# Performance work log

Measured on AMD Instinct MI355X. Metric: run time of the kernel, lower is better.

Reference implementation:

```python
import jax, jax.numpy as jnp
import numpy as np

N, D, G, H, M = 500000, 128, 64, 128, 256  # bag size, local_dim, global_dim, attn_hidden, mlp_hidden
TEMP = 1.0


def setup_inputs() -> dict:
    key = jax.random.key(0)
    ks = jax.random.split(key, 8)
    s = 0.05
    return {
        "bag": jax.random.normal(ks[0], (N, D), jnp.float32),
        "global_feat": jax.random.normal(ks[1], (G,), jnp.float32),
        # attention_V: Linear(D, H) + Tanh
        "Wv": jax.random.normal(ks[2], (H, D), jnp.float32) * s,
        "bv": jnp.zeros((H,), jnp.float32),
        # attention_U: Linear(D, H) + Sigmoid
        "Wu": jax.random.normal(ks[3], (H, D), jnp.float32) * s,
        "bu": jnp.zeros((H,), jnp.float32),
        # attention_weights: Linear(H, 1)
        "Ww": jax.random.normal(ks[4], (1, H), jnp.float32) * s,
        "bw": jnp.zeros((1,), jnp.float32),
        "W1": jax.random.normal(ks[5], (M, D + G), jnp.float32) * s,
        "b1": jnp.zeros((M,), jnp.float32),
        "W2": jax.random.normal(ks[6], (1, M), jnp.float32) * s,
        "b2": jnp.zeros((1,), jnp.float32),
    }


def reference(bag, global_feat, Wv, bv, Wu, bu, Ww, bw, W1, b1, W2, b2):
    # feature_extractor = Identity (use_feature_extractor=False); dropout = identity (eval)
    V = jnp.tanh(bag @ Wv.T + bv)            # [N, H]
    U = jax.nn.sigmoid(bag @ Wu.T + bu)      # [N, H]
    Ggate = V * U                            # [N, H]
    A_raw = Ggate @ Ww.T + bw                # [N, 1]
    alpha = jax.nn.softmax(A_raw / TEMP, axis=0)  # softmax over bag dim
    bag_embedding = alpha.T @ bag            # [1, D]
    fused = jnp.concatenate([bag_embedding, global_feat.reshape(1, -1)], axis=1)  # [1, D+G]
    h = jax.nn.leaky_relu(fused @ W1.T + b1, negative_slope=0.01)  # [1, M]
    score = h @ W2.T + b2                    # [1, 1]
    return (score, alpha)
```

## Files before the change

### kernel.cpp

```cpp
#include <hip/hip_runtime.h>
#include <hip/hip_bf16.h>

#define N_BAG 500000
#define DIM   128
#define ROWS_PER_ITER 32
#define ITERS 16
#define ROWS_PER_BLOCK 512
#define NBLK  977
#define GDIM  64
#define LDB   136

typedef __attribute__((ext_vector_type(8))) __bf16 bf16x8;
typedef __attribute__((ext_vector_type(4))) __bf16 bf16x4;
typedef __attribute__((ext_vector_type(4))) float  f32x4;

union BF8 { bf16x8 v; __bf16 e[8]; };

__device__ __forceinline__ float fast_rcp(float x) { return __builtin_amdgcn_rcpf(x); }

__global__ __launch_bounds__(256, 3)
void attn_pass1(const float* __restrict__ bag,
                const float* __restrict__ Wv, const float* __restrict__ bv,
                const float* __restrict__ Wu, const float* __restrict__ bu,
                const float* __restrict__ Ww, const float* __restrict__ bw,
                float* __restrict__ aOut,
                float* __restrict__ blkS, float* __restrict__ blkW,
                float* __restrict__ Eacc, float* __restrict__ Ssum)
{
    __shared__ __align__(16) unsigned char smem[2 * ROWS_PER_ITER * LDB * 2];
    __shared__ float a_part[ROWS_PER_ITER][4];

    typedef __bf16 XsRow[ROWS_PER_ITER][LDB];
    XsRow* Xs = (XsRow*)smem;
    float (*fin)[4] = (float(*)[4])smem;

    const int tid = threadIdx.x;
    const int w   = tid >> 6;
    const int L   = tid & 63;
    const int m16 = L & 15;
    const int q   = L >> 4;
    const int hh  = L >> 5;
    const int c32 = L & 31;
    const int blk = blockIdx.x;
    const int rowBase = blk * ROWS_PER_BLOCK;

    if (blk == 0) {
        if (tid < DIM) Eacc[tid] = 0.0f;
        if (tid == DIM) Ssum[0] = 0.0f;
    }

    BF8 fv[2][4], fu[2][4];
    float bvv[2], buu[2], www[2];
#pragma unroll
    for (int ht = 0; ht < 2; ++ht) {
        const int h = w*32 + ht*16 + m16;
        bvv[ht] = bv[h]; buu[ht] = bu[h]; www[ht] = Ww[h];
#pragma unroll
        for (int s = 0; s < 4; ++s) {
            const int d0 = s*32 + q*8;
            const float4 v0 = *(const float4*)(Wv + h*DIM + d0);
            const float4 v1 = *(const float4*)(Wv + h*DIM + d0 + 4);
            const float4 u0 = *(const float4*)(Wu + h*DIM + d0);
            const float4 u1 = *(const float4*)(Wu + h*DIM + d0 + 4);
            fv[ht][s].e[0]=(__bf16)v0.x; fv[ht][s].e[1]=(__bf16)v0.y;
            fv[ht][s].e[2]=(__bf16)v0.z; fv[ht][s].e[3]=(__bf16)v0.w;
            fv[ht][s].e[4]=(__bf16)v1.x; fv[ht][s].e[5]=(__bf16)v1.y;
            fv[ht][s].e[6]=(__bf16)v1.z; fv[ht][s].e[7]=(__bf16)v1.w;
            fu[ht][s].e[0]=(__bf16)u0.x; fu[ht][s].e[1]=(__bf16)u0.y;
            fu[ht][s].e[2]=(__bf16)u0.z; fu[ht][s].e[3]=(__bf16)u0.w;
            fu[ht][s].e[4]=(__bf16)u1.x; fu[ht][s].e[5]=(__bf16)u1.y;
            fu[ht][s].e[6]=(__bf16)u1.z; fu[ht][s].e[7]=(__bf16)u1.w;
        }
    }
    const float bw0 = bw[0];

    float4 stg[4];
#pragma unroll
    for (int i = 0; i < 4; ++i) {
        int r = rowBase + i*8 + w*2 + hh;
        if (r >= N_BAG) r = N_BAG - 1;
        stg[i] = *(const float4*)(bag + (size_t)r*DIM + c32*4);
    }

    float s_acc = 0.0f;
    float wacc0 = 0.f, wacc1 = 0.f, wacc2 = 0.f, wacc3 = 0.f;

    for (int it = 0; it < ITERS; ++it) {
        const int buf = it & 1;
        const int tileStart = rowBase + it*ROWS_PER_ITER;

#pragma unroll
        for (int i = 0; i < 4; ++i) {
            const int row = i*8 + w*2 + hh;
            bf16x4 pk;
            pk.x = (__bf16)stg[i].x; pk.y = (__bf16)stg[i].y;
            pk.z = (__bf16)stg[i].z; pk.w = (__bf16)stg[i].w;
            *(bf16x4*)&Xs[buf][row][c32*4] = pk;
        }
        __syncthreads();

        if (it + 1 < ITERS) {
            const int ts2 = tileStart + ROWS_PER_ITER;
#pragma unroll
            for (int i = 0; i < 4; ++i) {
                int r = ts2 + i*8 + w*2 + hh;
                if (r >= N_BAG) r = N_BAG - 1;
                stg[i] = *(const float4*)(bag + (size_t)r*DIM + c32*4);
            }
        }

#pragma unroll
        for (int r = 0; r < 2; ++r) {
            f32x4 accV[2], accU[2];
#pragma unroll
            for (int ht = 0; ht < 2; ++ht) {
                accV[ht] = (f32x4){0.f,0.f,0.f,0.f};
                accU[ht] = (f32x4){0.f,0.f,0.f,0.f};
            }
#pragma unroll
            for (int s = 0; s < 4; ++s) {
                const bf16x8 af = *(const bf16x8*)&Xs[buf][r*16 + m16][s*32 + q*8];
#pragma unroll
                for (int ht = 0; ht < 2; ++ht) {
                    accV[ht] = __builtin_amdgcn_mfma_f32_16x16x32_bf16(af, fv[ht][s].v, accV[ht], 0, 0, 0);
                    accU[ht] = __builtin_amdgcn_mfma_f32_16x16x32_bf16(af, fu[ht][s].v, accU[ht], 0, 0, 0);
                }
            }
            float psum[4];
#pragma unroll
            for (int g = 0; g < 4; ++g) {
                float p = 0.0f;
#pragma unroll
                for (int ht = 0; ht < 2; ++ht) {
                    const float z = accV[ht][g] + bvv[ht];
                    const float y = accU[ht][g] + buu[ht];
                    const float A = __expf(2.0f*z);
                    const float B = __expf(y);
                    p += (A - 1.0f) * B * www[ht] * fast_rcp((A + 1.0f) * (B + 1.0f));
                }
                p += __shfl_xor(p, 1); p += __shfl_xor(p, 2);
                p += __shfl_xor(p, 4); p += __shfl_xor(p, 8);
                psum[g] = p;
            }
            if (m16 == 0) {
#pragma unroll
                for (int g = 0; g < 4; ++g)
                    a_part[r*16 + q*4 + g][w] = psum[g];
            }
        }
        __syncthreads();

        const int li = L & 31;
        const float4 ap = *(const float4*)&a_part[li][0];
        float a = ap.x + ap.y + ap.z + ap.w + bw0;
        const int grow = tileStart + li;
        if (w == 0 && L < 32 && grow < N_BAG) aOut[grow] = a;
        if (grow >= N_BAG) a = -1e30f;
        const float e = __expf(a);
        if (L < 32) s_acc += e;

        float s0 = 0.f, s1 = 0.f, s2 = 0.f, s3 = 0.f;
#pragma unroll
        for (int i = 0; i < 4; ++i) {
            const int row = i*8 + w*2 + hh;
            const float ei = __shfl(e, row);
            const bf16x4 xb = *(const bf16x4*)&Xs[buf][row][c32*4];
            s0 += ei * (float)xb.x; s1 += ei * (float)xb.y;
            s2 += ei * (float)xb.z; s3 += ei * (float)xb.w;
        }
        wacc0 += s0; wacc1 += s1; wacc2 += s2; wacc3 += s3;
    }

    float st = s_acc;
    st += __shfl_xor(st, 1);  st += __shfl_xor(st, 2);
    st += __shfl_xor(st, 4);  st += __shfl_xor(st, 8);
    st += __shfl_xor(st, 16); st += __shfl_xor(st, 32);

    __syncthreads();
    fin[tid][0] = wacc0; fin[tid][1] = wacc1;
    fin[tid][2] = wacc2; fin[tid][3] = wacc3;
    if (L == 0) a_part[0][w] = st;
    __syncthreads();
    if (tid < 128) {
        float v = 0.0f;
#pragma unroll
        for (int k = 0; k < 8; ++k) {
            const int t = (k >> 1)*64 + (k & 1)*32 + (tid >> 2);
            v += fin[t][tid & 3];
        }
        blkW[blk*DIM + tid] = v;
    }
    if (tid == 0)
        blkS[blk] = a_part[0][0] + a_part[0][1] + a_part[0][2] + a_part[0][3];
}

__global__ void headA(const float* __restrict__ blkW, const float* __restrict__ blkS,
                      float* __restrict__ E, float* __restrict__ Ssum)
{
    const int tid = threadIdx.x;
    const int c = tid & 127, g = tid >> 7;
    const int b0 = blockIdx.x * 16;
    float acc = 0.0f;
#pragma unroll
    for (int t = 0; t < 8; ++t) {
        const int b = b0 + g*8 + t;
        if (b < NBLK) acc += blkW[b*DIM + c];
    }
    atomicAdd(&E[c], acc);

    if (tid < 16) {
        const int b = b0 + tid;
        float sv = (b < NBLK) ? blkS[b] : 0.0f;
        sv += __shfl_xor(sv, 1); sv += __shfl_xor(sv, 2);
        sv += __shfl_xor(sv, 4); sv += __shfl_xor(sv, 8);
        if (tid == 0) atomicAdd(Ssum, sv);
    }
}

__global__ void headB(const float* __restrict__ E, const float* __restrict__ Ssum,
                      const float* __restrict__ gfeat,
                      const float* __restrict__ W1, const float* __restrict__ b1,
                      const float* __restrict__ W2, const float* __restrict__ b2,
                      float* __restrict__ out)
{
    __shared__ float f[DIM + GDIM];
    __shared__ float red[256];
    const int tid = threadIdx.x;

    const float invS = 1.0f / Ssum[0];
    if (tid < DIM)             f[tid] = E[tid] * invS;
    else if (tid < DIM + GDIM) f[tid] = gfeat[tid - DIM];
    __syncthreads();

    float a2 = b1[tid];
    const float4* w1p = (const float4*)(W1 + tid * (DIM + GDIM));
    const float4* fp  = (const float4*)f;
#pragma unroll 4
    for (int k = 0; k < (DIM + GDIM) / 4; ++k) {
        const float4 a4 = w1p[k]; const float4 f4 = fp[k];
        a2 += a4.x*f4.x + a4.y*f4.y + a4.z*f4.z + a4.w*f4.w;
    }
    const float h = a2 > 0.0f ? a2 : 0.01f * a2;
    red[tid] = h * W2[tid]; __syncthreads();
    for (int s = 128; s > 0; s >>= 1) {
        if (tid < s) red[tid] += red[tid + s];
        __syncthreads();
    }
    if (tid == 0) out[0] = red[0] + b2[0];
}

__global__ void alpha_kernel(float* __restrict__ alpha, const float* __restrict__ Ssum)
{
    const int i = blockIdx.x * blockDim.x + threadIdx.x;
    const float invS = 1.0f / Ssum[0];
    if (i * 4 < N_BAG) {
        float4 a4 = *(float4*)(alpha + i*4);
        a4.x = __expf(a4.x) * invS; a4.y = __expf(a4.y) * invS;
        a4.z = __expf(a4.z) * invS; a4.w = __expf(a4.w) * invS;
        *(float4*)(alpha + i*4) = a4;
    }
}

extern "C" void kernel_launch(void* const* d_in, const int* in_sizes, int n_in,
                              void* d_out, int out_size, void* d_ws, size_t ws_size,
                              hipStream_t stream)
{
    const float* bag   = (const float*)d_in[0];
    const float* gfeat = (const float*)d_in[1];
    const float* Wv    = (const float*)d_in[2];
    const float* bv    = (const float*)d_in[3];
    const float* Wu    = (const float*)d_in[4];
    const float* bu    = (const float*)d_in[5];
    const float* Ww    = (const float*)d_in[6];
    const float* bw    = (const float*)d_in[7];
    const float* W1    = (const float*)d_in[8];
    const float* b1    = (const float*)d_in[9];
    const float* W2    = (const float*)d_in[10];
    const float* b2    = (const float*)d_in[11];
    float* out = (float*)d_out;
    float* ws  = (float*)d_ws;

    float* blkS = ws;
    float* blkW = ws + 1024;
    float* Eacc = ws + 1024 + 125056;
    float* Ssum = ws + 1024 + 125056 + 128;

    attn_pass1<<<NBLK, 256, 0, stream>>>(bag, Wv, bv, Wu, bu, Ww, bw,
                                         out + 1, blkS, blkW, Eacc, Ssum);
    headA<<<64, 256, 0, stream>>>(blkW, blkS, Eacc, Ssum);
    headB<<<1, 256, 0, stream>>>(Eacc, Ssum, gfeat, W1, b1, W2, b2, out);
    alpha_kernel<<<(N_BAG/4 + 255) / 256, 256, 0, stream>>>(out + 1, Ssum);
}
```

Baseline: 407.4 us.

## Double rows per pipeline step and fuse head reduction kernels into one

Each main-loop step of the attention pass now processes 64 rows instead of 32 in 8 steps. This halves the number of barriers and doubles the register-staged prefetch of bag rows. The two head kernels, which used atomics to combine block partials, are merged into one 1024-thread block that reduces all block partials in shared memory and computes the MLP score. That also removes the zero-initialisation of the accumulators in the main kernel. In exchange the main kernel needs more registers and LDS, which may lower occupancy, and the final reduction now runs on a single block.

```diff
diff --git a/kernel.cpp b/kernel.cpp
--- a/kernel.cpp
+++ b/kernel.cpp
@@ -3,8 +3,8 @@
 
 #define N_BAG 500000
 #define DIM   128
-#define ROWS_PER_ITER 32
-#define ITERS 16
+#define ROWS_PER_ITER 64
+#define ITERS 8
 #define ROWS_PER_BLOCK 512
 #define NBLK  977
 #define GDIM  64
@@ -24,11 +24,10 @@
                 const float* __restrict__ Wu, const float* __restrict__ bu,
                 const float* __restrict__ Ww, const float* __restrict__ bw,
                 float* __restrict__ aOut,
-                float* __restrict__ blkS, float* __restrict__ blkW,
-                float* __restrict__ Eacc, float* __restrict__ Ssum)
+                float* __restrict__ blkS, float* __restrict__ blkW)
 {
     __shared__ __align__(16) unsigned char smem[2 * ROWS_PER_ITER * LDB * 2];
-    __shared__ float a_part[ROWS_PER_ITER][4];
+    __shared__ __align__(16) float a_part[ROWS_PER_ITER][4];
 
     typedef __bf16 XsRow[ROWS_PER_ITER][LDB];
     XsRow* Xs = (XsRow*)smem;
@@ -43,11 +42,6 @@
     const int c32 = L & 31;
     const int blk = blockIdx.x;
     const int rowBase = blk * ROWS_PER_BLOCK;
-
-    if (blk == 0) {
-        if (tid < DIM) Eacc[tid] = 0.0f;
-        if (tid == DIM) Ssum[0] = 0.0f;
-    }
 
     BF8 fv[2][4], fu[2][4];
     float bvv[2], buu[2], www[2];
@@ -74,9 +68,9 @@
     }
     const float bw0 = bw[0];
 
-    float4 stg[4];
-#pragma unroll
-    for (int i = 0; i < 4; ++i) {
+    float4 stg[8];
+#pragma unroll
+    for (int i = 0; i < 8; ++i) {
         int r = rowBase + i*8 + w*2 + hh;
         if (r >= N_BAG) r = N_BAG - 1;
         stg[i] = *(const float4*)(bag + (size_t)r*DIM + c32*4);
@@ -90,7 +84,7 @@
         const int tileStart = rowBase + it*ROWS_PER_ITER;
 
 #pragma unroll
-        for (int i = 0; i < 4; ++i) {
+        for (int i = 0; i < 8; ++i) {
             const int row = i*8 + w*2 + hh;
             bf16x4 pk;
             pk.x = (__bf16)stg[i].x; pk.y = (__bf16)stg[i].y;
@@ -102,7 +96,7 @@
         if (it + 1 < ITERS) {
             const int ts2 = tileStart + ROWS_PER_ITER;
 #pragma unroll
-            for (int i = 0; i < 4; ++i) {
+            for (int i = 0; i < 8; ++i) {
                 int r = ts2 + i*8 + w*2 + hh;
                 if (r >= N_BAG) r = N_BAG - 1;
                 stg[i] = *(const float4*)(bag + (size_t)r*DIM + c32*4);
@@ -110,7 +104,7 @@
         }
 
 #pragma unroll
-        for (int r = 0; r < 2; ++r) {
+        for (int r = 0; r < 4; ++r) {
             f32x4 accV[2], accU[2];
 #pragma unroll
             for (int ht = 0; ht < 2; ++ht) {
@@ -150,18 +144,17 @@
         }
         __syncthreads();
 
-        const int li = L & 31;
-        const float4 ap = *(const float4*)&a_part[li][0];
+        const float4 ap = *(const float4*)&a_part[L][0];
         float a = ap.x + ap.y + ap.z + ap.w + bw0;
-        const int grow = tileStart + li;
-        if (w == 0 && L < 32 && grow < N_BAG) aOut[grow] = a;
+        const int grow = tileStart + L;
+        if (w == 0 && grow < N_BAG) aOut[grow] = a;
         if (grow >= N_BAG) a = -1e30f;
         const float e = __expf(a);
-        if (L < 32) s_acc += e;
+        if (w == 0) s_acc += e;
 
         float s0 = 0.f, s1 = 0.f, s2 = 0.f, s3 = 0.f;
 #pragma unroll
-        for (int i = 0; i < 4; ++i) {
+        for (int i = 0; i < 8; ++i) {
             const int row = i*8 + w*2 + hh;
             const float ei = __shfl(e, row);
             const bf16x4 xb = *(const bf16x4*)&Xs[buf][row][c32*4];
@@ -194,59 +187,63 @@
         blkS[blk] = a_part[0][0] + a_part[0][1] + a_part[0][2] + a_part[0][3];
 }
 
-__global__ void headA(const float* __restrict__ blkW, const float* __restrict__ blkS,
-                      float* __restrict__ E, float* __restrict__ Ssum)
-{
+__global__ __launch_bounds__(1024)
+void head_fused(const float* __restrict__ blkW, const float* __restrict__ blkS,
+                const float* __restrict__ gfeat,
+                const float* __restrict__ W1, const float* __restrict__ b1,
+                const float* __restrict__ W2, const float* __restrict__ b2,
+                float* __restrict__ out, float* __restrict__ Ssum)
+{
+    __shared__ float Ered[8][DIM];
+    __shared__ float Sred[16];
+    __shared__ __align__(16) float f[DIM + GDIM];
+    __shared__ float red4[4];
     const int tid = threadIdx.x;
-    const int c = tid & 127, g = tid >> 7;
-    const int b0 = blockIdx.x * 16;
+    const int g = tid >> 7, c = tid & 127;
+
     float acc = 0.0f;
-#pragma unroll
-    for (int t = 0; t < 8; ++t) {
-        const int b = b0 + g*8 + t;
-        if (b < NBLK) acc += blkW[b*DIM + c];
-    }
-    atomicAdd(&E[c], acc);
-
-    if (tid < 16) {
-        const int b = b0 + tid;
-        float sv = (b < NBLK) ? blkS[b] : 0.0f;
-        sv += __shfl_xor(sv, 1); sv += __shfl_xor(sv, 2);
-        sv += __shfl_xor(sv, 4); sv += __shfl_xor(sv, 8);
-        if (tid == 0) atomicAdd(Ssum, sv);
-    }
-}
-
-__global__ void headB(const float* __restrict__ E, const float* __restrict__ Ssum,
-                      const float* __restrict__ gfeat,
-                      const float* __restrict__ W1, const float* __restrict__ b1,
-                      const float* __restrict__ W2, const float* __restrict__ b2,
-                      float* __restrict__ out)
-{
-    __shared__ float f[DIM + GDIM];
-    __shared__ float red[256];
-    const int tid = threadIdx.x;
-
-    const float invS = 1.0f / Ssum[0];
-    if (tid < DIM)             f[tid] = E[tid] * invS;
-    else if (tid < DIM + GDIM) f[tid] = gfeat[tid - DIM];
-    __syncthreads();
-
-    float a2 = b1[tid];
-    const float4* w1p = (const float4*)(W1 + tid * (DIM + GDIM));
-    const float4* fp  = (const float4*)f;
+    for (int b = g; b < NBLK; b += 8) acc += blkW[b*DIM + c];
+    Ered[g][c] = acc;
+
+    float sv = (tid < NBLK) ? blkS[tid] : 0.0f;
+    sv += __shfl_xor(sv, 1);  sv += __shfl_xor(sv, 2);
+    sv += __shfl_xor(sv, 4);  sv += __shfl_xor(sv, 8);
+    sv += __shfl_xor(sv, 16); sv += __shfl_xor(sv, 32);
+    if ((tid & 63) == 0) Sred[tid >> 6] = sv;
+    __syncthreads();
+
+    if (tid < DIM) {
+        float S = 0.0f;
+#pragma unroll
+        for (int k = 0; k < 16; ++k) S += Sred[k];
+        float E = 0.0f;
+#pragma unroll
+        for (int k = 0; k < 8; ++k) E += Ered[k][tid];
+        f[tid] = E / S;
+        if (tid == 0) Ssum[0] = S;
+    } else if (tid < DIM + GDIM) {
+        f[tid] = gfeat[tid - DIM];
+    }
+    __syncthreads();
+
+    if (tid < 256) {
+        float a2 = b1[tid];
+        const float4* w1p = (const float4*)(W1 + tid * (DIM + GDIM));
+        const float4* fp  = (const float4*)f;
 #pragma unroll 4
-    for (int k = 0; k < (DIM + GDIM) / 4; ++k) {
-        const float4 a4 = w1p[k]; const float4 f4 = fp[k];
-        a2 += a4.x*f4.x + a4.y*f4.y + a4.z*f4.z + a4.w*f4.w;
-    }
-    const float h = a2 > 0.0f ? a2 : 0.01f * a2;
-    red[tid] = h * W2[tid]; __syncthreads();
-    for (int s = 128; s > 0; s >>= 1) {
-        if (tid < s) red[tid] += red[tid + s];
-        __syncthreads();
-    }
-    if (tid == 0) out[0] = red[0] + b2[0];
+        for (int k = 0; k < (DIM + GDIM) / 4; ++k) {
+            const float4 a4 = w1p[k]; const float4 f4 = fp[k];
+            a2 += a4.x*f4.x + a4.y*f4.y + a4.z*f4.z + a4.w*f4.w;
+        }
+        const float h = a2 > 0.0f ? a2 : 0.01f * a2;
+        float p = h * W2[tid];
+        p += __shfl_xor(p, 1);  p += __shfl_xor(p, 2);
+        p += __shfl_xor(p, 4);  p += __shfl_xor(p, 8);
+        p += __shfl_xor(p, 16); p += __shfl_xor(p, 32);
+        if ((tid & 63) == 0) red4[tid >> 6] = p;
+    }
+    __syncthreads();
+    if (tid == 0) out[0] = red4[0] + red4[1] + red4[2] + red4[3] + b2[0];
 }
 
 __global__ void alpha_kernel(float* __restrict__ alpha, const float* __restrict__ Ssum)
@@ -282,12 +279,10 @@
 
     float* blkS = ws;
     float* blkW = ws + 1024;
-    float* Eacc = ws + 1024 + 125056;
-    float* Ssum = ws + 1024 + 125056 + 128;
+    float* Ssum = ws + 1024 + 125056;
 
     attn_pass1<<<NBLK, 256, 0, stream>>>(bag, Wv, bv, Wu, bu, Ww, bw,
-                                         out + 1, blkS, blkW, Eacc, Ssum);
-    headA<<<64, 256, 0, stream>>>(blkW, blkS, Eacc, Ssum);
-    headB<<<1, 256, 0, stream>>>(Eacc, Ssum, gfeat, W1, b1, W2, b2, out);
+                                         out + 1, blkS, blkW);
+    head_fused<<<1, 1024, 0, stream>>>(blkW, blkS, gfeat, W1, b1, W2, b2, out, Ssum);
     alpha_kernel<<<(N_BAG/4 + 255) / 256, 256, 0, stream>>>(out + 1, Ssum);
 }
```

Measured after the change: 426.4 us. 4.7% more time.
